# Performance work log

Hardware: AMD Instinct MI355X
Metric: run time of the kernel (lower is better)

## Reference

```python
import jax, jax.numpy as jnp
import numpy as np

B, H, W = 1, 180, 360
NB, BS = 8, 96
EMBED = NB * BS            # 768
LATENT = 4 * EMBED         # 3072 (mlp_ratio=4)
MODD = 64
LAM = 0.01                 # sparsity_threshold (softshrink)

def _ln(x, w, b):
    m = x.mean(-1, keepdims=True)
    v = x.var(-1, keepdims=True)
    return (x - m) * jax.lax.rsqrt(v + 1e-5) * w + b

def _gelu(x):
    return jax.nn.gelu(x, approximate=False)  # torch nn.GELU default (erf)

def _scale_shift(e, w0, b0, w1, b1):
    o = _gelu(e @ w0 + b0) @ w1 + b1
    s, t = jnp.split(o, 2, axis=1)
    return 1.0 + s, t

def _softshrink(x):
    return jnp.where(x > LAM, x - LAM, jnp.where(x < -LAM, x + LAM, 0.0))

def _bd(x, w):  # block-diagonal contraction on spectral features
    return jnp.einsum('nyxbi,bio->nyxbo', x, w)

def _filter(x, e, w1, b1, w2, b2, fs_w0, fs_b0, fs_w1, fs_b1):
    bias = x
    b, h, w, c = x.shape
    xf = jnp.fft.rfft2(x, axes=(1, 2), norm='ortho')
    wf = w // 2 + 1
    xr = xf.real.reshape(b, h, wf, NB, BS)
    xi = xf.imag.reshape(b, h, wf, NB, BS)
    tm = min(h, w) // 2 + 1
    km = tm  # hard_thresholding_fraction = 1.0
    lo, hi = tm - km, min(tm + km, h)
    xrk, xik = xr[:, lo:hi, :km], xi[:, lo:hi, :km]
    o1r = _bd(xrk, w1[0]) - _bd(xik, w1[1]) + b1[0]
    o1i = _bd(xik, w1[0]) + _bd(xrk, w1[1]) + b1[1]
    s, t = _scale_shift(e, fs_w0, fs_b0, fs_w1, fs_b1)  # 'real' mode
    s = s.reshape(b, 1, 1, NB, BS)
    t = t.reshape(b, 1, 1, NB, BS)
    o1r = jax.nn.relu(o1r * s + t)
    o1i = jax.nn.relu(o1i * s + t)
    o2r = _softshrink(_bd(o1r, w2[0]) - _bd(o1i, w2[1]) + b2[0])
    o2i = _softshrink(_bd(o1i, w2[0]) + _bd(o1r, w2[1]) + b2[1])
    full = jnp.zeros((b, h, wf, NB, BS), jnp.complex64)
    full = full.at[:, lo:hi, :km].set(o2r + 1j * o2i)
    out = jnp.fft.irfft2(full.reshape(b, h, wf, c), s=(h, w), axes=(1, 2), norm='ortho')
    return out + bias

def _mlp(x, e, fc1w, fc1b, fc2w, fc2b, ms_w0, ms_b0, ms_w1, ms_b1):
    s, t = _scale_shift(e, ms_w0, ms_b0, ms_w1, ms_b1)
    s = s[:, None, None, :]
    t = t[:, None, None, :]
    hmid = _gelu((x @ fc1w + fc1b) * s + t)
    return hmid @ fc2w + fc2b

def setup_inputs():
    key = jax.random.key(0)
    ks = jax.random.split(key, 16)
    g = lambda k, shp: 0.02 * jax.random.normal(k, shp, jnp.float32)
    return {
        'x': jax.random.normal(ks[0], (B, H, W, EMBED), jnp.float32),
        'mod_embed': jax.random.normal(ks[1], (B, MODD), jnp.float32),
        'n1w': jnp.ones((EMBED,), jnp.float32),
        'n1b': jnp.zeros((EMBED,), jnp.float32),
        'n2w': jnp.ones((EMBED,), jnp.float32),
        'n2b': jnp.zeros((EMBED,), jnp.float32),
        'w1': g(ks[2], (2, NB, BS, BS)),
        'b1': g(ks[3], (2, NB, BS)),
        'w2': g(ks[4], (2, NB, BS, BS)),
        'b2': g(ks[5], (2, NB, BS)),
        'fs_w0': g(ks[6], (MODD, 2 * EMBED)),
        'fs_b0': jnp.zeros((2 * EMBED,), jnp.float32),
        'fs_w1': g(ks[7], (2 * EMBED, 2 * EMBED)),
        'fs_b1': jnp.zeros((2 * EMBED,), jnp.float32),
        'fc1w': g(ks[8], (EMBED, LATENT)),
        'fc1b': jnp.zeros((LATENT,), jnp.float32),
        'fc2w': g(ks[9], (LATENT, EMBED)),
        'fc2b': jnp.zeros((EMBED,), jnp.float32),
        'ms_w0': g(ks[10], (MODD, 2 * LATENT)),
        'ms_b0': jnp.zeros((2 * LATENT,), jnp.float32),
        'ms_w1': g(ks[11], (2 * LATENT, 2 * LATENT)),
        'ms_b1': jnp.zeros((2 * LATENT,), jnp.float32),
    }

def reference(x, mod_embed, n1w, n1b, n2w, n2b, w1, b1, w2, b2,
              fs_w0, fs_b0, fs_w1, fs_b1, fc1w, fc1b, fc2w, fc2b,
              ms_w0, ms_b0, ms_w1, ms_b1):
    residual = x
    h = _ln(x, n1w, n1b)
    h = _filter(h, mod_embed, w1, b1, w2, b2, fs_w0, fs_b0, fs_w1, fs_b1)
    h = h + residual            # double_skip = True
    residual = h
    h2 = _ln(h, n2w, n2b)
    h2 = _mlp(h2, mod_embed, fc1w, fc1b, fc2w, fc2b, ms_w0, ms_b0, ms_w1, ms_b1)
    return h2 + residual
```

## Files before the change

kernel.cpp:

```cpp
#include <hip/hip_runtime.h>
#include <hip/hip_bf16.h>
#include <math.h>

#define HH 180
#define WW 360
#define CC 768
#define FF 91
#define NPOS (HH*FF)
#define NROW (HH*WW)
#define LAT 3072

typedef __attribute__((ext_vector_type(8))) short bf16x8;
typedef __attribute__((ext_vector_type(4))) float f32x4;
typedef __attribute__((ext_vector_type(4))) unsigned int u32x4;

__device__ __forceinline__ float gelu_f(float x) {
    return 0.5f * x * (1.0f + erff(x * 0.7071067811865476f));
}

__global__ __launch_bounds__(256) void mod_a_kernel(
        const float* __restrict__ e,
        const float* __restrict__ fs_w0, const float* __restrict__ fs_b0,
        const float* __restrict__ ms_w0, const float* __restrict__ ms_b0,
        float* __restrict__ mid_f, float* __restrict__ mid_m) {
    __shared__ float es[64];
    int t = threadIdx.x;
    if (t < 64) es[t] = e[t];
    __syncthreads();
    int j = blockIdx.x * 256 + t;
    if (j < 1536) {
        float a = fs_b0[j];
        #pragma unroll 8
        for (int k = 0; k < 64; k++) a += es[k] * fs_w0[k*1536 + j];
        mid_f[j] = gelu_f(a);
    } else {
        int jm = j - 1536;
        float a = ms_b0[jm];
        #pragma unroll 8
        for (int k = 0; k < 64; k++) a += es[k] * ms_w0[k*6144 + jm];
        mid_m[jm] = gelu_f(a);
    }
}

__global__ __launch_bounds__(512) void mod_b_kernel(
        const float* __restrict__ mid_f, const float* __restrict__ mid_m,
        const float* __restrict__ fs_w1, const float* __restrict__ fs_b1,
        const float* __restrict__ ms_w1, const float* __restrict__ ms_b1,
        float* __restrict__ s_f, float* __restrict__ t_f,
        float* __restrict__ s_m, float* __restrict__ t_m) {
    __shared__ float red[8*64];
    int t = threadIdx.x;
    int g = t >> 6;
    int jl = t & 63;
    int blk = blockIdx.x;
    if (blk < 24) {
        int jo = blk*64 + jl;
        const int N = 1536, NQ = 192;
        float a = 0.f;
        const float* w = fs_w1 + (size_t)(g*NQ)*N + jo;
        for (int j = 0; j < NQ; j++) a += mid_f[g*NQ + j] * w[(size_t)j*N];
        red[t] = a;
        __syncthreads();
        if (t < 64) {
            float s = fs_b1[jo];
            #pragma unroll
            for (int q = 0; q < 8; q++) s += red[q*64 + jl];
            if (jo < 768) s_f[jo] = 1.0f + s;
            else          t_f[jo - 768] = s;
        }
    } else {
        int jo = (blk - 24)*64 + jl;
        const int N = 6144, NQ = 768;
        float a = 0.f;
        const float* w = ms_w1 + (size_t)(g*NQ)*N + jo;
        for (int j = 0; j < NQ; j++) a += mid_m[g*NQ + j] * w[(size_t)j*N];
        red[t] = a;
        __syncthreads();
        if (t < 64) {
            float s = ms_b1[jo];
            #pragma unroll
            for (int q = 0; q < 8; q++) s += red[q*64 + jl];
            if (jo < 3072) s_m[jo] = 1.0f + s;
            else           t_m[jo - 3072] = s;
        }
    }
}

__global__ __launch_bounds__(256) void ln_bf16_kernel(const float* __restrict__ in,
        const float* __restrict__ w, const float* __restrict__ b,
        __hip_bfloat16* __restrict__ out) {
    int row = blockIdx.x*4 + (threadIdx.x >> 6);
    int l = threadIdx.x & 63;
    const float* p = in + (size_t)row*CC;
    float v[12]; float s = 0.f, sq = 0.f;
    #pragma unroll
    for (int i = 0; i < 12; i++) { float tv = p[l + 64*i]; v[i] = tv; s += tv; sq += tv*tv; }
    #pragma unroll
    for (int m = 1; m < 64; m <<= 1) { s += __shfl_xor(s, m); sq += __shfl_xor(sq, m); }
    float mean = s * (1.0f/768.0f);
    float var  = sq * (1.0f/768.0f) - mean*mean;
    float rstd = rsqrtf(var + 1e-5f);
    __hip_bfloat16* o = out + (size_t)row*CC;
    #pragma unroll
    for (int i = 0; i < 12; i++) { int c = l + 64*i; o[c] = __float2bfloat16((v[i]-mean)*rstd*w[c] + b[c]); }
}

__global__ __launch_bounds__(256) void ew_kernel(__hip_bfloat16* __restrict__ Ew) {
    int idx = blockIdx.x*256 + threadIdx.x;
    if (idx >= 192*384) return;
    int r = idx / 384, w = idx - (idx/384)*384;
    int f = (r < 96) ? r : r - 96;
    const float rn = 0.05270462766947299f;
    float v = 0.f;
    if (f < FF && w < WW) {
        int p = (f * w) % 360;
        float ang = 6.283185307179586f/360.0f * (float)p;
        float s_, c_; sincosf(ang, &s_, &c_);
        v = (r < 96) ? c_*rn : -s_*rn;
    }
    Ew[idx] = __float2bfloat16(v);
}

__global__ __launch_bounds__(256) void eh_kernel(__hip_bfloat16* __restrict__ Eh) {
    int idx = blockIdx.x*256 + threadIdx.x;
    if (idx >= 4*192*384) return;
    int sp = idx / (192*384);
    int rem = idx - sp*(192*384);
    int t = rem / 384, k = rem - (rem/384)*384;
    int sig = sp >> 1, plane = sp & 1;
    float s = (sig == 0) ? -1.f : 1.f;
    int h = (k < 192) ? k : k - 192;
    const float rnh = 0.07453559924999299f;
    float v = 0.f;
    if (t < HH && h < HH) {
        int p = (t * h) % 180;
        float ang = 6.283185307179586f/180.0f * (float)p;
        float s_, c_; sincosf(ang, &s_, &c_);
        float C = c_*rnh, S = s_*rnh;
        if (plane == 0) v = (k < 192) ? C : -s*S;
        else            v = (k < 192) ? s*S : C;
    }
    Eh[idx] = __float2bfloat16(v);
}

__global__ __launch_bounds__(256) void bdw_kernel(const float* __restrict__ w,
        __hip_bfloat16* __restrict__ Bt) {
    int idx = blockIdx.x*256 + threadIdx.x;
    if (idx >= 8*192*192) return;
    int wb = idx / (192*192);
    int rem = idx - wb*(192*192);
    int n2 = rem / 192, k2 = rem - (rem/192)*192;
    int k = (k2 < 96) ? k2 : k2 - 96;
    int oc = (n2 < 96) ? n2 : n2 - 96;
    float w0 = w[((size_t)wb*96 + k)*96 + oc];
    float w1v = w[((size_t)(8 + wb)*96 + k)*96 + oc];
    float v;
    if (n2 < 96) v = (k2 < 96) ? w0 : -w1v;
    else         v = (k2 < 96) ? w1v : w0;
    Bt[idx] = __float2bfloat16(v);
}

template<int MODE>
__global__ __launch_bounds__(256) void transform_mfma(
        const __hip_bfloat16* __restrict__ Amat,
        const __hip_bfloat16* __restrict__ B0, const __hip_bfloat16* __restrict__ B1,
        __hip_bfloat16* __restrict__ O0, __hip_bfloat16* __restrict__ O1) {
    __shared__ __align__(16) unsigned short As[192*72];
    __shared__ __align__(16) unsigned short Bs[128*72];
    int nbase = blockIdx.x * 128;
    int bat = blockIdx.z;
    int tid = threadIdx.x;
    int l = tid & 63, wv = tid >> 6;
    int wm = wv & 1, wn = wv >> 1;
    int lm = l & 15, kq = l >> 4;
    const __hip_bfloat16* Ab = Amat + (MODE == 1 ? (size_t)blockIdx.y*192*384 : 0);
    f32x4 acc[6][4] = {};
    for (int kt = 0; kt < 6; kt++) {
        int kb = kt*64;
        __syncthreads();
        #pragma unroll
        for (int it = 0; it < 6; it++) {
            int ch = it*256 + tid;
            int row = ch >> 3, co = (ch & 7) * 8;
            u32x4 v = *(const u32x4*)(Ab + (size_t)row*384 + kb + co);
            *(u32x4*)(As + row*72 + co) = v;
        }
        #pragma unroll
        for (int it = 0; it < 4; it++) {
            int idx = it*256 + tid;
            int row = idx >> 4;
            int cq = (idx & 15) * 8;
            int k = kb + row;
            unsigned int u[4] = {0u, 0u, 0u, 0u};
            if (MODE == 0) {
                if (k < WW) {
                    u32x4 v = *(const u32x4*)(B0 + (size_t)bat*WW*CC + (size_t)k*CC + nbase + cq);
                    u[0] = v[0]; u[1] = v[1]; u[2] = v[2]; u[3] = v[3];
                }
            } else {
                if (k < 192) {
                    if (k < HH) {
                        u32x4 v = *(const u32x4*)(B0 + (size_t)k*FF*CC + (size_t)bat*CC + nbase + cq);
                        u[0] = v[0]; u[1] = v[1]; u[2] = v[2]; u[3] = v[3];
                    }
                } else {
                    int h2 = k - 192;
                    if (h2 < HH) {
                        u32x4 v = *(const u32x4*)(B1 + (size_t)h2*FF*CC + (size_t)bat*CC + nbase + cq);
                        u[0] = v[0]; u[1] = v[1]; u[2] = v[2]; u[3] = v[3];
                    }
                }
            }
            #pragma unroll
            for (int j = 0; j < 4; j++) {
                Bs[(cq + 2*j    )*72 + row] = (unsigned short)(u[j] & 0xffffu);
                Bs[(cq + 2*j + 1)*72 + row] = (unsigned short)(u[j] >> 16);
            }
        }
        __syncthreads();
        #pragma unroll
        for (int kk = 0; kk < 2; kk++) {
            int kg = kk*32 + kq*8;
            bf16x8 af[6], bfv[4];
            #pragma unroll
            for (int i = 0; i < 6; i++)
                af[i] = *(const bf16x8*)(As + (wm*96 + i*16 + lm)*72 + kg);
            #pragma unroll
            for (int j = 0; j < 4; j++)
                bfv[j] = *(const bf16x8*)(Bs + (wn*64 + j*16 + lm)*72 + kg);
            #pragma unroll
            for (int i = 0; i < 6; i++)
                #pragma unroll
                for (int j = 0; j < 4; j++)
                    acc[i][j] = __builtin_amdgcn_mfma_f32_16x16x32_bf16(af[i], bfv[j], acc[i][j], 0, 0, 0);
        }
    }
    int r0 = kq * 4;
    #pragma unroll
    for (int j = 0; j < 4; j++) {
        int col = nbase + wn*64 + j*16 + lm;
        #pragma unroll
        for (int i = 0; i < 6; i++) {
            #pragma unroll
            for (int r = 0; r < 4; r++) {
                int row = wm*96 + i*16 + r0 + r;
                __hip_bfloat16 hv = __float2bfloat16(acc[i][j][r]);
                if (MODE == 0) {
                    if (row < 96) {
                        if (row < FF) O0[(size_t)bat*FF*CC + (size_t)row*CC + col] = hv;
                    } else {
                        int f2 = row - 96;
                        if (f2 < FF) O1[(size_t)bat*FF*CC + (size_t)f2*CC + col] = hv;
                    }
                } else {
                    if (row < HH) {
                        __hip_bfloat16* Op = blockIdx.y ? O1 : O0;
                        Op[(size_t)row*FF*CC + (size_t)bat*CC + col] = hv;
                    }
                }
            }
        }
    }
}

template<int LAYER>
__global__ __launch_bounds__(384) void bd_mfma_kernel(
        const __hip_bfloat16* __restrict__ Ir, const __hip_bfloat16* __restrict__ Ii,
        const __hip_bfloat16* __restrict__ Bt,
        const float* __restrict__ bias,
        const float* __restrict__ sf, const float* __restrict__ tf,
        __hip_bfloat16* __restrict__ Or_, __hip_bfloat16* __restrict__ Oi_) {
    __shared__ __align__(16) unsigned short As[128*72];
    __shared__ __align__(16) unsigned short Bs[192*72];
    int mbase = blockIdx.x * 128;
    int wb = blockIdx.y;
    int tid = threadIdx.x;
    int l = tid & 63, wv = tid >> 6;
    int wm = wv & 1, wn = wv >> 1;
    int lm = l & 15, kq = l >> 4;
    const __hip_bfloat16* Bw = Bt + (size_t)wb*192*192;
    f32x4 acc[4][4] = {};
    for (int kt = 0; kt < 3; kt++) {
        __syncthreads();
        for (int ch = tid; ch < 1024; ch += 384) {
            int row = ch >> 3, q = ch & 7;
            int k2 = kt*64 + q*8;
            int p = mbase + row; if (p >= NPOS) p = NPOS - 1;
            const __hip_bfloat16* src = (k2 < 96) ? (Ir + (size_t)p*CC + wb*96 + k2)
                                                  : (Ii + (size_t)p*CC + wb*96 + (k2 - 96));
            *(u32x4*)(As + row*72 + q*8) = *(const u32x4*)src;
        }
        for (int ch = tid; ch < 1536; ch += 384) {
            int row = ch >> 3, co = (ch & 7) * 8;
            u32x4 v = *(const u32x4*)(Bw + (size_t)row*192 + kt*64 + co);
            *(u32x4*)(Bs + row*72 + co) = v;
        }
        __syncthreads();
        #pragma unroll
        for (int kk = 0; kk < 2; kk++) {
            int kg = kk*32 + kq*8;
            bf16x8 af[4], bfv[4];
            #pragma unroll
            for (int i = 0; i < 4; i++) {
                af[i]  = *(const bf16x8*)(As + (wm*64 + i*16 + lm)*72 + kg);
                bfv[i] = *(const bf16x8*)(Bs + (wn*64 + i*16 + lm)*72 + kg);
            }
            #pragma unroll
            for (int i = 0; i < 4; i++)
                #pragma unroll
                for (int j = 0; j < 4; j++)
                    acc[i][j] = __builtin_amdgcn_mfma_f32_16x16x32_bf16(af[i], bfv[j], acc[i][j], 0, 0, 0);
        }
    }
    int r0 = kq * 4;
    #pragma unroll
    for (int j = 0; j < 4; j++) {
        int n2 = wn*64 + j*16 + lm;
        int oc = (n2 < 96) ? n2 : n2 - 96;
        float bb = bias[((n2 < 96) ? 0 : 768) + wb*96 + oc];
        float ss = 0.f, tt = 0.f;
        if (LAYER == 0) { ss = sf[wb*96 + oc]; tt = tf[wb*96 + oc]; }
        __hip_bfloat16* Op = (n2 < 96) ? Or_ : Oi_;
        #pragma unroll
        for (int i = 0; i < 4; i++) {
            #pragma unroll
            for (int r = 0; r < 4; r++) {
                int p = mbase + wm*64 + i*16 + r0 + r;
                if (p < NPOS) {
                    float v = acc[i][j][r] + bb;
                    if (LAYER == 0) {
                        v = fmaxf(v*ss + tt, 0.0f);
                    } else {
                        v = (v > 0.01f) ? (v - 0.01f) : ((v < -0.01f) ? (v + 0.01f) : 0.0f);
                    }
                    Op[(size_t)p*CC + wb*96 + oc] = __float2bfloat16(v);
                }
            }
        }
    }
}

__global__ __launch_bounds__(256) void aw_kernel(__hip_bfloat16* __restrict__ Aw) {
    int idx = blockIdx.x*256 + threadIdx.x;
    if (idx >= 384*96) return;
    int w = idx / 96, f = idx - (idx/96)*96;
    const float rn = 0.05270462766947299f;
    float m = (f == 0) ? rn : ((f < FF) ? 2.0f*rn : 0.0f);
    int p = (int)(((long long)f * w) % 360);
    float ang = 6.283185307179586f / 360.0f * (float)p;
    float s_, c_; sincosf(ang, &s_, &c_);
    Aw[idx]          = __float2bfloat16(m * c_);
    Aw[384*96 + idx] = __float2bfloat16(-m * s_);
}

__global__ __launch_bounds__(256) void iwdft_mfma_kernel(
        const __hip_bfloat16* __restrict__ Zr, const __hip_bfloat16* __restrict__ Zi,
        const __hip_bfloat16* __restrict__ Aw,
        const __hip_bfloat16* __restrict__ hlnb,
        const float* __restrict__ xin, float* __restrict__ hout) {
    __shared__ __align__(16) unsigned short As[128*104];
    __shared__ __align__(16) unsigned short Bs[128*104];
    int h = blockIdx.z;
    int mbase = blockIdx.y * 128;
    int nbase = blockIdx.x * 128;
    int tid = threadIdx.x;
    int l = tid & 63, wv = tid >> 6;
    int wm = wv & 1, wn = wv >> 1;
    int lm = l & 15, kq = l >> 4;
    f32x4 acc[4][4] = {};
    #pragma unroll
    for (int ph = 0; ph < 2; ph++) {
        __syncthreads();
        for (int ch = tid; ch < 1536; ch += 256) {
            int row = ch / 12, co = (ch - row*12) * 8;
            u32x4 v = *(const u32x4*)(Aw + ((size_t)ph*384 + mbase + row)*96 + co);
            *(u32x4*)(As + row*104 + co) = v;
        }
        const __hip_bfloat16* Zp = ph ? Zi : Zr;
        for (int ch = tid; ch < 1536; ch += 256) {
            int f = ch >> 4, cq = (ch & 15) * 8;
            unsigned int u[4] = {0u, 0u, 0u, 0u};
            if (f < FF) {
                u32x4 v = *(const u32x4*)(Zp + ((size_t)h*FF + f)*CC + nbase + cq);
                u[0] = v[0]; u[1] = v[1]; u[2] = v[2]; u[3] = v[3];
            }
            #pragma unroll
            for (int j = 0; j < 4; j++) {
                Bs[(cq + 2*j    )*104 + f] = (unsigned short)(u[j] & 0xffffu);
                Bs[(cq + 2*j + 1)*104 + f] = (unsigned short)(u[j] >> 16);
            }
        }
        __syncthreads();
        #pragma unroll
        for (int ks = 0; ks < 3; ks++) {
            int kg = ks*32 + kq*8;
            bf16x8 af[4], bfv[4];
            #pragma unroll
            for (int i = 0; i < 4; i++) {
                af[i]  = *(const bf16x8*)(As + (wm*64 + i*16 + lm)*104 + kg);
                bfv[i] = *(const bf16x8*)(Bs + (wn*64 + i*16 + lm)*104 + kg);
            }
            #pragma unroll
            for (int i = 0; i < 4; i++)
                #pragma unroll
                for (int j = 0; j < 4; j++)
                    acc[i][j] = __builtin_amdgcn_mfma_f32_16x16x32_bf16(af[i], bfv[j], acc[i][j], 0, 0, 0);
        }
    }
    int r0 = kq * 4;
    #pragma unroll
    for (int j = 0; j < 4; j++) {
        int col = nbase + wn*64 + j*16 + lm;
        #pragma unroll
        for (int i = 0; i < 4; i++) {
            int rowb = wm*64 + i*16 + r0;
            #pragma unroll
            for (int r = 0; r < 4; r++) {
                int wp = mbase + rowb + r;
                if (wp < WW) {
                    size_t idx = ((size_t)h*WW + wp)*CC + col;
                    hout[idx] = acc[i][j][r] + __bfloat162float(hlnb[idx]) + xin[idx];
                }
            }
        }
    }
}

__global__ __launch_bounds__(256) void transpose_bf16_kernel(const float* __restrict__ src,
        __hip_bfloat16* __restrict__ dst, int K, int N) {
    __shared__ float tile[32][33];
    int n0 = blockIdx.x * 32;
    int k0 = blockIdx.y * 32;
    int tx = threadIdx.x & 31;
    int ty = threadIdx.x >> 5;
    #pragma unroll
    for (int r = 0; r < 32; r += 8) {
        tile[ty + r][tx] = src[(size_t)(k0 + ty + r) * N + n0 + tx];
    }
    __syncthreads();
    #pragma unroll
    for (int r = 0; r < 32; r += 8) {
        dst[(size_t)(n0 + ty + r) * K + k0 + tx] = __float2bfloat16(tile[tx][ty + r]);
    }
}

template<int MODE>
__global__ __launch_bounds__(512, 2) void gemm256_kernel(
        const __hip_bfloat16* __restrict__ A,
        const __hip_bfloat16* __restrict__ Bt,
        int M, int K, int N,
        const float* __restrict__ bias,
        const float* __restrict__ sv, const float* __restrict__ tv,
        const float* resid, void* out) {
    __shared__ __align__(16) unsigned short SH[65536];
    unsigned short* Asb = SH;
    unsigned short* Bsb = SH + 32768;
    int tid = threadIdx.x;
    int nbase = blockIdx.x * 256;
    int mbase = blockIdx.y * 256;
    int l = tid & 63, wv = tid >> 6;
    int wm = wv & 1, wn = wv >> 1;
    int lm = l & 15, kq = l >> 4;
    f32x4 acc[8][4] = {};
    int nkt = K >> 6;

    auto stage = [&](int d, int kt) {
        int kb = kt << 6;
        #pragma unroll
        for (int i = 0; i < 4; i++) {
            int ch = i*512 + tid;
            int row = ch >> 3;
            int sl = ch & 7;
            int kg = (sl ^ (row & 7)) << 3;
            int am = mbase + row; if (am >= M) am = M - 1;
            const __hip_bfloat16* ga = A  + (size_t)am * K + kb + kg;
            const __hip_bfloat16* gb = Bt + (size_t)(nbase + row) * K + kb + kg;
            __builtin_amdgcn_global_load_lds(
                (const __attribute__((address_space(1))) void*)(unsigned long long)(uintptr_t)ga,
                (__attribute__((address_space(3))) void*)(unsigned long long)(uintptr_t)(Asb + d*16384 + ch*8),
                16, 0, 0);
            __builtin_amdgcn_global_load_lds(
                (const __attribute__((address_space(1))) void*)(unsigned long long)(uintptr_t)gb,
                (__attribute__((address_space(3))) void*)(unsigned long long)(uintptr_t)(Bsb + d*16384 + ch*8),
                16, 0, 0);
        }
    };

    stage(0, 0);
    __syncthreads();
    for (int kt = 0; kt < nkt; kt++) {
        if (kt + 1 < nkt) stage((kt + 1) & 1, kt + 1);
        int d = kt & 1;
        const unsigned short* Ab = Asb + d*16384;
        const unsigned short* Bb = Bsb + d*16384;
        #pragma unroll
        for (int kk = 0; kk < 2; kk++) {
            bf16x8 af[8], bfv[4];
            #pragma unroll
            for (int i = 0; i < 8; i++) {
                int ra = wm*128 + i*16 + lm;
                af[i] = *(const bf16x8*)(Ab + ra*64 + ((((kk<<2)+kq) ^ (ra&7))<<3));
            }
            #pragma unroll
            for (int j = 0; j < 4; j++) {
                int rb = wn*64 + j*16 + lm;
                bfv[j] = *(const bf16x8*)(Bb + rb*64 + ((((kk<<2)+kq) ^ (rb&7))<<3));
            }
            #pragma unroll
            for (int i = 0; i < 8; i++)
                #pragma unroll
                for (int j = 0; j < 4; j++)
                    acc[i][j] = __builtin_amdgcn_mfma_f32_16x16x32_bf16(af[i], bfv[j], acc[i][j], 0, 0, 0);
        }
        __syncthreads();
    }

    int r0 = kq * 4;
    if (MODE == 0) {
        #pragma unroll
        for (int j = 0; j < 4; j++) {
            int col = wn*64 + j*16 + lm;
            int gcol = nbase + col;
            float bb = bias[gcol];
            float ss = sv[gcol], tt = tv[gcol];
            #pragma unroll
            for (int i = 0; i < 8; i++) {
                int rowb = wm*128 + i*16 + r0;
                #pragma unroll
                for (int r = 0; r < 4; r++) {
                    float v = gelu_f((acc[i][j][r] + bb)*ss + tt);
                    __hip_bfloat16 hb = __float2bfloat16(v);
                    SH[(rowb + r)*256 + col] = *reinterpret_cast<unsigned short*>(&hb);
                }
            }
        }
        __syncthreads();
        #pragma unroll
        for (int it = 0; it < 16; it++) {
            int chunk = it*512 + tid;
            int row = chunk >> 5;
            int c8 = chunk & 31;
            int mr = mbase + row;
            if (mr < M) {
                *(u32x4*)((__hip_bfloat16*)out + (size_t)mr*N + nbase + c8*8) =
                    *(const u32x4*)(SH + row*256 + c8*8);
            }
        }
    } else {
        #pragma unroll
        for (int j = 0; j < 4; j++) {
            int col = nbase + wn*64 + j*16 + lm;
            float bb = bias[col];
            #pragma unroll
            for (int i = 0; i < 8; i++) {
                int rowb = mbase + wm*128 + i*16 + r0;
                #pragma unroll
                for (int r = 0; r < 4; r++) {
                    int row = rowb + r;
                    if (row < M) {
                        float v = acc[i][j][r] + bb;
                        ((float*)out)[(size_t)row*N + col] = v + resid[(size_t)row*N + col];
                    }
                }
            }
        }
    }
}

extern "C" void kernel_launch(void* const* d_in, const int* in_sizes, int n_in,
                              void* d_out, int out_size, void* d_ws, size_t ws_size,
                              hipStream_t stream) {
    const float* x     = (const float*)d_in[0];
    const float* emb   = (const float*)d_in[1];
    const float* n1w   = (const float*)d_in[2];
    const float* n1b   = (const float*)d_in[3];
    const float* n2w   = (const float*)d_in[4];
    const float* n2b   = (const float*)d_in[5];
    const float* w1    = (const float*)d_in[6];
    const float* b1    = (const float*)d_in[7];
    const float* w2    = (const float*)d_in[8];
    const float* b2    = (const float*)d_in[9];
    const float* fs_w0 = (const float*)d_in[10];
    const float* fs_b0 = (const float*)d_in[11];
    const float* fs_w1 = (const float*)d_in[12];
    const float* fs_b1 = (const float*)d_in[13];
    const float* fc1w  = (const float*)d_in[14];
    const float* fc1b  = (const float*)d_in[15];
    const float* fc2w  = (const float*)d_in[16];
    const float* fc2b  = (const float*)d_in[17];
    const float* ms_w0 = (const float*)d_in[18];
    const float* ms_b0 = (const float*)d_in[19];
    const float* ms_w1 = (const float*)d_in[20];
    const float* ms_b1 = (const float*)d_in[21];
    float* out = (float*)d_out;
    (void)in_sizes; (void)n_in; (void)out_size; (void)ws_size;

    char* wsb = (char*)d_ws;
    size_t off = 0;
    auto alloc = [&](size_t nbytes) -> void* {
        void* p = wsb + off;
        off += (nbytes + 255) & ~(size_t)255;
        return p;
    };
    float* s_f  = (float*)alloc(768*4);
    float* t_f  = (float*)alloc(768*4);
    float* s_m  = (float*)alloc(3072*4);
    float* t_m  = (float*)alloc(3072*4);
    float* midf = (float*)alloc(1536*4);
    float* midm = (float*)alloc(6144*4);
    __hip_bfloat16* Aw  = (__hip_bfloat16*)alloc((size_t)2*384*96*2);
    __hip_bfloat16* Ew  = (__hip_bfloat16*)alloc((size_t)192*384*2);
    __hip_bfloat16* Eh  = (__hip_bfloat16*)alloc((size_t)4*192*384*2);
    __hip_bfloat16* Bt1 = (__hip_bfloat16*)alloc((size_t)8*192*192*2);
    __hip_bfloat16* Bt2 = (__hip_bfloat16*)alloc((size_t)8*192*192*2);
    __hip_bfloat16* Yrb = (__hip_bfloat16*)alloc((size_t)NPOS*CC*2);
    __hip_bfloat16* Yib = (__hip_bfloat16*)alloc((size_t)NPOS*CC*2);
    __hip_bfloat16* Zrb = (__hip_bfloat16*)alloc((size_t)NPOS*CC*2);
    __hip_bfloat16* Zib = (__hip_bfloat16*)alloc((size_t)NPOS*CC*2);
    __hip_bfloat16* wT1  = (__hip_bfloat16*)alloc((size_t)CC*LAT*2);
    __hip_bfloat16* wT2  = (__hip_bfloat16*)alloc((size_t)CC*LAT*2);
    __hip_bfloat16* h2   = (__hip_bfloat16*)alloc((size_t)NROW*CC*2);
    __hip_bfloat16* hmid = (__hip_bfloat16*)alloc((size_t)NROW*LAT*2);
    __hip_bfloat16* hlnb = h2;

    mod_a_kernel<<<30, 256, 0, stream>>>(emb, fs_w0, fs_b0, ms_w0, ms_b0, midf, midm);
    mod_b_kernel<<<120, 512, 0, stream>>>(midf, midm, fs_w1, fs_b1, ms_w1, ms_b1,
                                          s_f, t_f, s_m, t_m);
    aw_kernel<<<144, 256, 0, stream>>>(Aw);
    ew_kernel<<<288, 256, 0, stream>>>(Ew);
    eh_kernel<<<1152, 256, 0, stream>>>(Eh);
    bdw_kernel<<<1152, 256, 0, stream>>>(w1, Bt1);
    bdw_kernel<<<1152, 256, 0, stream>>>(w2, Bt2);
    ln_bf16_kernel<<<NROW/4, 256, 0, stream>>>(x, n1w, n1b, hlnb);
    transpose_bf16_kernel<<<dim3(LAT/32, CC/32), 256, 0, stream>>>(fc1w, wT1, 768, 3072);
    transpose_bf16_kernel<<<dim3(CC/32, LAT/32), 256, 0, stream>>>(fc2w, wT2, 3072, 768);

    transform_mfma<0><<<dim3(6, 1, 180), 256, 0, stream>>>(Ew, hlnb, nullptr, Yrb, Yib);
    transform_mfma<1><<<dim3(6, 2, 91), 256, 0, stream>>>(Eh, Yrb, Yib, Zrb, Zib);
    bd_mfma_kernel<0><<<dim3(128, 8), 384, 0, stream>>>(Zrb, Zib, Bt1, b1, s_f, t_f, Yrb, Yib);
    bd_mfma_kernel<1><<<dim3(128, 8), 384, 0, stream>>>(Yrb, Yib, Bt2, b2, nullptr, nullptr, Zrb, Zib);
    transform_mfma<1><<<dim3(6, 2, 91), 256, 0, stream>>>(Eh + (size_t)2*192*384, Zrb, Zib, Yrb, Yib);
    iwdft_mfma_kernel<<<dim3(6, 3, 180), 256, 0, stream>>>(Yrb, Yib, Aw, hlnb, x, out);

    ln_bf16_kernel<<<NROW/4, 256, 0, stream>>>(out, n2w, n2b, h2);
    gemm256_kernel<0><<<dim3(LAT/256, (NROW+255)/256), 512, 0, stream>>>(
        h2, wT1, NROW, CC, LAT, fc1b, s_m, t_m, nullptr, hmid);
    gemm256_kernel<1><<<dim3(CC/256, (NROW+255)/256), 512, 0, stream>>>(
        hmid, wT2, NROW, LAT, CC, fc2b, nullptr, nullptr, out, out);
}
```

Before: 1.940 ms.

## Split GEMM k-tile into four phases with fine-grained vmcnt waits and setprio

Restructures the main bf16 MFMA GEMM loop so that each k-tile is computed in four phases, each covering two A row-groups. Next-tile global-to-LDS loads are interleaved across the phases, and explicit s_waitcnt vmcnt counts let each phase wait only for the rows it needs. s_setprio is raised around the MFMA bursts. The aim is finer overlap of loads with compute instead of a full barrier per tile. The cost is more barriers per tile and correctness that depends on the hand-counted vmcnt values.

```diff
diff --git a/kernel.cpp b/kernel.cpp
--- a/kernel.cpp
+++ b/kernel.cpp
@@ -464,56 +464,85 @@
     f32x4 acc[8][4] = {};
     int nkt = K >> 6;
 
-    auto stage = [&](int d, int kt) {
+    auto gload = [&](const __hip_bfloat16* g, unsigned short* lds) {
+        __builtin_amdgcn_global_load_lds(
+            (const __attribute__((address_space(1))) void*)(unsigned long long)(uintptr_t)g,
+            (__attribute__((address_space(3))) void*)(unsigned long long)(uintptr_t)lds,
+            16, 0, 0);
+    };
+    auto stageB = [&](int d, int kt, int half) {
         int kb = kt << 6;
         #pragma unroll
-        for (int i = 0; i < 4; i++) {
-            int ch = i*512 + tid;
+        for (int i = 0; i < 2; i++) {
+            int ch = half*1024 + i*512 + tid;
             int row = ch >> 3;
             int sl = ch & 7;
             int kg = (sl ^ (row & 7)) << 3;
-            int am = mbase + row; if (am >= M) am = M - 1;
-            const __hip_bfloat16* ga = A  + (size_t)am * K + kb + kg;
-            const __hip_bfloat16* gb = Bt + (size_t)(nbase + row) * K + kb + kg;
-            __builtin_amdgcn_global_load_lds(
-                (const __attribute__((address_space(1))) void*)(unsigned long long)(uintptr_t)ga,
-                (__attribute__((address_space(3))) void*)(unsigned long long)(uintptr_t)(Asb + d*16384 + ch*8),
-                16, 0, 0);
-            __builtin_amdgcn_global_load_lds(
-                (const __attribute__((address_space(1))) void*)(unsigned long long)(uintptr_t)gb,
-                (__attribute__((address_space(3))) void*)(unsigned long long)(uintptr_t)(Bsb + d*16384 + ch*8),
-                16, 0, 0);
+            gload(Bt + (size_t)(nbase + row) * K + kb + kg, Bsb + d*16384 + ch*8);
         }
     };
-
-    stage(0, 0);
-    __syncthreads();
+    auto stageA = [&](int d, int kt, int p) {
+        int kb = kt << 6;
+        int rl = tid >> 3;
+        int row = (rl < 32) ? (p*32 + rl) : (96 + p*32 + rl);
+        int sl = tid & 7;
+        int kg = (sl ^ (row & 7)) << 3;
+        int am = mbase + row; if (am >= M) am = M - 1;
+        gload(A + (size_t)am * K + kb + kg, Asb + d*16384 + row*64 + sl*8);
+    };
+
+#define GPHASE(P, VM, STAGECODE)                                                          \
+    {                                                                                     \
+        STAGECODE;                                                                        \
+        asm volatile("s_waitcnt vmcnt(" #VM ")" ::: "memory");                            \
+        __builtin_amdgcn_s_barrier();                                                     \
+        asm volatile("" ::: "memory");                                                    \
+        int ra0 = wm*128 + (2*(P))*16 + lm;                                               \
+        int ra1 = ra0 + 16;                                                               \
+        bf16x8 a00 = *(const bf16x8*)(Ab + ra0*64 + (((kq    ) ^ (ra0&7))<<3));           \
+        bf16x8 a01 = *(const bf16x8*)(Ab + ra0*64 + (((4 + kq) ^ (ra0&7))<<3));           \
+        bf16x8 a10 = *(const bf16x8*)(Ab + ra1*64 + (((kq    ) ^ (ra1&7))<<3));           \
+        bf16x8 a11 = *(const bf16x8*)(Ab + ra1*64 + (((4 + kq) ^ (ra1&7))<<3));           \
+        bf16x8 bv[4][2];                                                                  \
+        _Pragma("unroll")                                                                 \
+        for (int j = 0; j < 4; j++) {                                                     \
+            int rb = wn*64 + j*16 + lm;                                                   \
+            bv[j][0] = *(const bf16x8*)(Bb + rb*64 + (((kq    ) ^ (rb&7))<<3));           \
+            bv[j][1] = *(const bf16x8*)(Bb + rb*64 + (((4 + kq) ^ (rb&7))<<3));           \
+        }                                                                                 \
+        __builtin_amdgcn_s_setprio(1);                                                    \
+        _Pragma("unroll")                                                                 \
+        for (int j = 0; j < 4; j++) {                                                     \
+            acc[2*(P)][j]   = __builtin_amdgcn_mfma_f32_16x16x32_bf16(a00, bv[j][0], acc[2*(P)][j],   0,0,0); \
+            acc[2*(P)][j]   = __builtin_amdgcn_mfma_f32_16x16x32_bf16(a01, bv[j][1], acc[2*(P)][j],   0,0,0); \
+            acc[2*(P)+1][j] = __builtin_amdgcn_mfma_f32_16x16x32_bf16(a10, bv[j][0], acc[2*(P)+1][j], 0,0,0); \
+            acc[2*(P)+1][j] = __builtin_amdgcn_mfma_f32_16x16x32_bf16(a11, bv[j][1], acc[2*(P)+1][j], 0,0,0); \
+        }                                                                                 \
+        __builtin_amdgcn_s_setprio(0);                                                    \
+    }
+
+    stageB(0, 0, 0); stageB(0, 0, 1);
+    stageA(0, 0, 0); stageA(0, 0, 1); stageA(0, 0, 2); stageA(0, 0, 3);
     for (int kt = 0; kt < nkt; kt++) {
-        if (kt + 1 < nkt) stage((kt + 1) & 1, kt + 1);
         int d = kt & 1;
         const unsigned short* Ab = Asb + d*16384;
         const unsigned short* Bb = Bsb + d*16384;
-        #pragma unroll
-        for (int kk = 0; kk < 2; kk++) {
-            bf16x8 af[8], bfv[4];
-            #pragma unroll
-            for (int i = 0; i < 8; i++) {
-                int ra = wm*128 + i*16 + lm;
-                af[i] = *(const bf16x8*)(Ab + ra*64 + ((((kk<<2)+kq) ^ (ra&7))<<3));
-            }
-            #pragma unroll
-            for (int j = 0; j < 4; j++) {
-                int rb = wn*64 + j*16 + lm;
-                bfv[j] = *(const bf16x8*)(Bb + rb*64 + ((((kk<<2)+kq) ^ (rb&7))<<3));
-            }
-            #pragma unroll
-            for (int i = 0; i < 8; i++)
-                #pragma unroll
-                for (int j = 0; j < 4; j++)
-                    acc[i][j] = __builtin_amdgcn_mfma_f32_16x16x32_bf16(af[i], bfv[j], acc[i][j], 0, 0, 0);
-        }
-        __syncthreads();
-    }
+        if (kt + 1 < nkt) {
+            int dn = d ^ 1, kn = kt + 1;
+            GPHASE(0, 5, stageB(dn, kn, 0))
+            GPHASE(1, 6, stageB(dn, kn, 1))
+            GPHASE(2, 7, stageA(dn, kn, 0); stageA(dn, kn, 1))
+            GPHASE(3, 8, stageA(dn, kn, 2); stageA(dn, kn, 3))
+        } else {
+            GPHASE(0, 3, (void)0)
+            GPHASE(1, 2, (void)0)
+            GPHASE(2, 1, (void)0)
+            GPHASE(3, 0, (void)0)
+        }
+        asm volatile("" ::: "memory");
+        __builtin_amdgcn_s_barrier();
+    }
+#undef GPHASE
 
     int r0 = kq * 4;
     if (MODE == 0) {
```

Result: slower. 4.041 ms (+108.3%).
